# Kernel tuning notes

Measured on AMD Instinct MI355X. Metric: run time of the kernel, lower is better.

The kernel has to match this reference:

```python
import jax, jax.numpy as jnp
import numpy as np

B, C_IN, P, N = 4, 8, 12000, 64
C_PFN = 64          # PFN output channels (hardcoded in source)
H = W = 282         # BEV canvas size (hardcoded)
PILLAR = 0.16       # pillar size in meters
XMIN = YMIN = -22.0 # grid origin (x_edges/y_edges = arange(-22, 22, 0.16))
EPS = 1e-5          # BatchNorm eps (torch default)


def setup_inputs() -> dict:
    key = jax.random.key(0)
    ks = jax.random.split(key, 12)
    # coordinates/features uniform in the grid range so pillars land on the canvas
    sweep = jax.random.uniform(ks[0], (B, C_IN, P, N), jnp.float32, -22.0, 22.0)
    map_in = jax.random.uniform(ks[1], (B, C_IN, P, N), jnp.float32, -22.0, 22.0)
    s = 1.0 / np.sqrt(C_IN)
    w_sweep = jax.random.uniform(ks[2], (C_PFN, C_IN), jnp.float32, -s, s)
    b_sweep = jax.random.uniform(ks[3], (C_PFN,), jnp.float32, -s, s)
    gamma_sweep = 1.0 + 0.1 * jax.random.normal(ks[4], (C_PFN,), jnp.float32)
    beta_sweep = 0.1 * jax.random.normal(ks[5], (C_PFN,), jnp.float32)
    w_map = jax.random.uniform(ks[6], (C_PFN, C_IN), jnp.float32, -s, s)
    b_map = jax.random.uniform(ks[7], (C_PFN,), jnp.float32, -s, s)
    gamma_map = 1.0 + 0.1 * jax.random.normal(ks[8], (C_PFN,), jnp.float32)
    beta_map = 0.1 * jax.random.normal(ks[9], (C_PFN,), jnp.float32)
    sbb = 1.0 / np.sqrt(2 * C_PFN)
    w_bb = jax.random.uniform(ks[10], (C_PFN, 2 * C_PFN), jnp.float32, -sbb, sbb)
    b_bb = jax.random.uniform(ks[11], (C_PFN,), jnp.float32, -sbb, sbb)
    return {"sweep": sweep, "map_in": map_in,
            "w_sweep": w_sweep, "b_sweep": b_sweep,
            "gamma_sweep": gamma_sweep, "beta_sweep": beta_sweep,
            "w_map": w_map, "b_map": b_map,
            "gamma_map": gamma_map, "beta_map": beta_map,
            "w_bb": w_bb, "b_bb": b_bb}


def pfn(x, w, b, gamma, beta):
    # 1x1 conv: [B,8,P,N] -> [B,64,P,N]
    y = jnp.einsum('bcpn,oc->bopn', x, w) + b[None, :, None, None]
    # BatchNorm2d, training-mode batch stats over (B,P,N) per channel
    mean = y.mean(axis=(0, 2, 3), keepdims=True)
    var = y.var(axis=(0, 2, 3), keepdims=True)
    y = (y - mean) * jax.lax.rsqrt(var + EPS)
    y = y * gamma[None, :, None, None] + beta[None, :, None, None]
    y = jax.nn.relu(y)
    return y.max(axis=3)  # max over points -> [B,64,P]


def scatter_to_canvas(inp, feats):
    # inp: [B,8,P,N] (x,y coords at channels 0,1, point 0); feats: [B,64,P]
    x = inp[:, 0, :, 0]  # [B,P]
    y = inp[:, 1, :, 0]
    valid = x != 0  # pillar_list = nonzero(PFN_input[b,0,:,0])
    xg = jnp.clip(jnp.floor((x - XMIN) / PILLAR).astype(jnp.int32), 0, W - 1)
    yg = jnp.clip(jnp.floor((y - YMIN) / PILLAR).astype(jnp.int32), 0, H - 1)
    # route invalid pillars out of bounds so mode='drop' discards them
    xg = jnp.where(valid, xg, W)
    yg = jnp.where(valid, yg, H)
    bidx = jnp.broadcast_to(jnp.arange(B, dtype=jnp.int32)[:, None], (B, P))
    canvas = jnp.zeros((B, H, W, C_PFN), feats.dtype)
    canvas = canvas.at[bidx, yg, xg].set(jnp.swapaxes(feats, 1, 2), mode='drop')
    return jnp.transpose(canvas, (0, 3, 1, 2))  # [B,64,H,W]


def reference(sweep, map_in, w_sweep, b_sweep, gamma_sweep, beta_sweep,
              w_map, b_map, gamma_map, beta_map, w_bb, b_bb):
    sweep_feats = pfn(sweep, w_sweep, b_sweep, gamma_sweep, beta_sweep)
    map_feats = pfn(map_in, w_map, b_map, gamma_map, beta_map)
    sweep_canvas = scatter_to_canvas(sweep, sweep_feats)
    map_canvas = scatter_to_canvas(map_in, map_feats)
    cat = jnp.concatenate([sweep_canvas, map_canvas], axis=1)  # [B,128,H,W]
    # Backbone 1x1 conv (in-channels corrected to 128 to match the data)
    out = jnp.einsum('bchw,oc->bohw', cat, w_bb) + b_bb[None, :, None, None]
    return out
```

## Files before the change

### kernel.cpp

```cpp
#include <hip/hip_runtime.h>
#include <cfloat>
#include <math.h>

namespace {
constexpr int Bn = 4, Cin = 8, Pn = 12000, Nn = 64, Co = 64, Hh = 282, Ww = 282;
constexpr int NPIL  = Bn * Pn;
constexpr int NCELL = Hh * Ww;
constexpr int CHW   = Pn * Nn;
constexpr double CNTD = (double)Bn * Pn * Nn;
constexpr int K1B = 1024;
constexpr int WL_CAP = 48000;
constexpr int APPLY_B = (WL_CAP + 255) / 256;
constexpr int FILL_B = (Bn * Co * NCELL / 4) / 256;

constexpr size_t PAR_OFF  = 0;
constexpr size_t MOM_OFF  = 1024;
constexpr size_t HDR_OFF  = 2048;
constexpr size_t WLS_OFF  = 8192;
constexpr size_t PART_OFF = WLS_OFF;
constexpr size_t WLM_OFF  = WLS_OFF + (size_t)WL_CAP * 8;
constexpr size_t WIN_OFF  = WLM_OFF + (size_t)WL_CAP * 8;
constexpr size_t YMAX_OFF = WIN_OFF + (size_t)2 * Bn * NCELL * 4;
constexpr size_t WS_NEED  = YMAX_OFF + (size_t)2 * NPIL * 64 * 4;

typedef __attribute__((ext_vector_type(8))) float f32x8_t;

__device__ __forceinline__ int cell_of(float xc, float yc) {
  int xg = (int)floorf((xc + 22.0f) * 6.25f);
  int yg = (int)floorf((yc + 22.0f) * 6.25f);
  xg = min(max(xg, 0), Ww - 1);
  yg = min(max(yg, 0), Hh - 1);
  return yg * Ww + xg;
}

__device__ __forceinline__ float firstlane(float v) {
  return __int_as_float(__builtin_amdgcn_readfirstlane(__float_as_int(v)));
}

__device__ __forceinline__ float dpp_xor1(float v) {
  return __int_as_float(__builtin_amdgcn_update_dpp(
      0, __float_as_int(v), 0xB1, 0xF, 0xF, true));
}
__device__ __forceinline__ float dpp_xor2(float v) {
  return __int_as_float(__builtin_amdgcn_update_dpp(
      0, __float_as_int(v), 0x4E, 0xF, 0xF, true));
}
}

__global__ void kdiag(float* __restrict__ out, float v) {
  if (threadIdx.x == 0 && blockIdx.x == 0) out[0] = v;
}

__global__ __launch_bounds__(256) void kinit_fill(
    const float* __restrict__ b_bb, float* __restrict__ out,
    int* __restrict__ winners, int* __restrict__ hdr)
{
  if (blockIdx.x < FILL_B) {
    const int idx = blockIdx.x * 256 + threadIdx.x;
    const int plane = idx / (NCELL / 4);
    const float v = b_bb[plane & 63];
    ((float4*)out)[idx] = make_float4(v, v, v, v);
  } else {
    const int t = (blockIdx.x - FILL_B) * 256 + threadIdx.x;
    if (t < 8) hdr[t] = 0;
    for (int i = t; i < 2 * Bn * NCELL; i += 256 * 256) winners[i] = -1;
  }
}

__global__ __launch_bounds__(256) void k1_momfeat(
    const float* __restrict__ sweep, const float* __restrict__ map_in,
    const float* __restrict__ w_s, const float* __restrict__ b_s,
    const float* __restrict__ w_m, const float* __restrict__ b_m,
    float* __restrict__ partOut, int* __restrict__ winners,
    float* __restrict__ ymax)
{
  __shared__ float red[4][44];
  const int lane = threadIdx.x & 63;
  const int wv   = threadIdx.x >> 6;
  const int bid2 = blockIdx.x & (K1B - 1);
  const int inp  = blockIdx.x / K1B;
  const float* x  = inp ? map_in : sweep;
  const float* w  = inp ? w_m : w_s;
  const float* bb = inp ? b_m : b_s;
  int*   win = winners + inp * Bn * NCELL;
  float* ym  = ymax + (size_t)inp * NPIL * 64;
  const int gw   = (bid2 * 256 + (int)threadIdx.x) >> 6;
  const int nw   = (K1B * 256) >> 6;

  float sacc[8];
  float macc[36];
#pragma unroll
  for (int i = 0; i < 8; ++i) sacc[i] = 0.f;
#pragma unroll
  for (int i = 0; i < 36; ++i) macc[i] = 0.f;

  const int l0 = lane & 1, l1 = (lane >> 1) & 1, l2 = (lane >> 2) & 1;

  for (int pp = gw; pp < NPIL; pp += nw) {
    const int b = pp / Pn;
    const int p = pp - b * Pn;
    const float* xb = x + (size_t)b * Cin * CHW + (size_t)p * Nn + lane;
    float xv[Cin];
#pragma unroll
    for (int c = 0; c < Cin; ++c) xv[c] = xb[(size_t)c * CHW];

#pragma unroll
    for (int c = 0; c < Cin; ++c) sacc[c] += xv[c];
    {
      int k = 0;
#pragma unroll
      for (int i = 0; i < 8; ++i)
#pragma unroll
        for (int j = i; j < 8; ++j) { macc[k] = fmaf(xv[i], xv[j], macc[k]); ++k; }
    }

    const float xc = firstlane(xv[0]);
    if (xc != 0.0f) {
      const float yc = firstlane(xv[1]);
      if (lane == 0) atomicMax(&win[b * NCELL + cell_of(xc, yc)], p);
    }

    float res = 0.f;
#pragma unroll
    for (int g = 0; g < 8; ++g) {
      f32x8_t wr0, wr1, wr2, wr3, wr4, wr5, wr6, wr7, b8;
      asm("s_load_dwordx8 %0, %9, 0x0\n\t"
          "s_load_dwordx8 %1, %9, 0x20\n\t"
          "s_load_dwordx8 %2, %9, 0x40\n\t"
          "s_load_dwordx8 %3, %9, 0x60\n\t"
          "s_load_dwordx8 %4, %9, 0x80\n\t"
          "s_load_dwordx8 %5, %9, 0xA0\n\t"
          "s_load_dwordx8 %6, %9, 0xC0\n\t"
          "s_load_dwordx8 %7, %9, 0xE0\n\t"
          "s_load_dwordx8 %8, %10, 0x0\n\t"
          "s_waitcnt lgkmcnt(0)"
          : "=&s"(wr0), "=&s"(wr1), "=&s"(wr2), "=&s"(wr3), "=&s"(wr4),
            "=&s"(wr5), "=&s"(wr6), "=&s"(wr7), "=&s"(b8)
          : "s"(w + g * 64), "s"(bb + g * 8));

      float z[8];
#define PFN_ROW(J, WR)                                                        \
      {                                                                       \
        float y = b8[J];                                                      \
        _Pragma("unroll")                                                     \
        for (int c = 0; c < Cin; ++c) y = fmaf(WR[c], xv[c], y);              \
        z[J] = y;                                                             \
      }
      PFN_ROW(0, wr0) PFN_ROW(1, wr1) PFN_ROW(2, wr2) PFN_ROW(3, wr3)
      PFN_ROW(4, wr4) PFN_ROW(5, wr5) PFN_ROW(6, wr6) PFN_ROW(7, wr7)
#undef PFN_ROW

      float t0[4];
#pragma unroll
      for (int i = 0; i < 4; ++i) {
        const float send = l0 ? z[2 * i] : z[2 * i + 1];
        const float keep = l0 ? z[2 * i + 1] : z[2 * i];
        t0[i] = fmaxf(keep, dpp_xor1(send));
      }
      float t1[2];
#pragma unroll
      for (int i = 0; i < 2; ++i) {
        const float send = l1 ? t0[2 * i] : t0[2 * i + 1];
        const float keep = l1 ? t0[2 * i + 1] : t0[2 * i];
        t1[i] = fmaxf(keep, dpp_xor2(send));
      }
      {
        const float send = l2 ? t1[0] : t1[1];
        const float keep = l2 ? t1[1] : t1[0];
        float v = fmaxf(keep, __shfl_xor(send, 4, 64));
        v = fmaxf(v, __shfl_xor(v, 8, 64));
        v = fmaxf(v, __shfl_xor(v, 16, 64));
        v = fmaxf(v, __shfl_xor(v, 32, 64));
        if ((lane >> 3) == g) res = v;
      }
    }
    ym[(size_t)pp * 64 + lane] = res;
  }

#pragma unroll
  for (int k = 0; k < 44; ++k) {
    float v = (k < 8) ? sacc[k] : macc[k - 8];
#pragma unroll
    for (int off = 32; off > 0; off >>= 1) v += __shfl_down(v, off, 64);
    if (lane == 0) red[wv][k] = v;
  }
  __syncthreads();
  if (threadIdx.x < 44) {
    const float s = red[0][threadIdx.x] + red[1][threadIdx.x] +
                    red[2][threadIdx.x] + red[3][threadIdx.x];
    partOut[(size_t)bid2 * 88 + inp * 44 + threadIdx.x] = s;
  }
}

__global__ __launch_bounds__(256) void k1b_reduce(
    const float* __restrict__ part, double* __restrict__ mom)
{
  __shared__ double sd[256];
  const int t = blockIdx.x;
  double s = 0.0;
  for (int blk = threadIdx.x; blk < K1B; blk += 256)
    s += (double)part[(size_t)blk * 88 + t];
  sd[threadIdx.x] = s;
  __syncthreads();
  for (int off = 128; off > 0; off >>= 1) {
    if (threadIdx.x < off) sd[threadIdx.x] += sd[threadIdx.x + off];
    __syncthreads();
  }
  if (threadIdx.x == 0) mom[t] = sd[0];
}

__global__ void k2_params(const double* __restrict__ mom,
    const float* __restrict__ w_s, const float* __restrict__ b_s,
    const float* __restrict__ g_s, const float* __restrict__ be_s,
    const float* __restrict__ w_m, const float* __restrict__ b_m,
    const float* __restrict__ g_m, const float* __restrict__ be_m,
    float* __restrict__ par, int* __restrict__ hdr)
{
  const int t = threadIdx.x;
  if (t >= 128) return;
  const int inp = t >> 6, o = t & 63;
  const double* m = mom + inp * 44;
  const float* w    = (inp ? w_m : w_s) + o * Cin;
  const float bias  = (inp ? b_m : b_s)[o];
  const float gamma = (inp ? g_m : g_s)[o];
  const float beta  = (inp ? be_m : be_s)[o];
  double S[8];
#pragma unroll
  for (int c = 0; c < 8; ++c) S[c] = m[c] / CNTD;
  double mean = (double)bias;
#pragma unroll
  for (int c = 0; c < 8; ++c) mean += (double)w[c] * S[c];
  double var = 0.0;
  int k = 8;
#pragma unroll
  for (int i = 0; i < 8; ++i)
#pragma unroll
    for (int j = i; j < 8; ++j) {
      const double cov = m[k] / CNTD - S[i] * S[j];
      const double ww = (double)w[i] * (double)w[j];
      var += (i == j ? ww : 2.0 * ww) * cov;
      ++k;
    }
  const double a = (double)gamma / sqrt(var + 1e-5);
  const double c = (double)beta - mean * a;
  const float af = (float)a;
  par[inp * 128 + o]      = af;
  par[inp * 128 + 64 + o] = (float)c;
  if (af < 0.f) atomicOr(&hdr[4 + inp * 2 + (o >> 5)], 1 << (o & 31));
}

__global__ __launch_bounds__(256) void k_negfix(
    const float* __restrict__ sweep, const float* __restrict__ map_in,
    const float* __restrict__ w_s, const float* __restrict__ b_s,
    const float* __restrict__ w_m, const float* __restrict__ b_m,
    const int* __restrict__ hdr, float* __restrict__ ymax)
{
  const int inp = blockIdx.x & 1;
  const unsigned m0 = (unsigned)hdr[4 + inp * 2];
  const unsigned m1 = (unsigned)hdr[5 + inp * 2];
  if ((m0 | m1) == 0u) return;
  const float* x  = inp ? map_in : sweep;
  const float* w  = inp ? w_m : w_s;
  const float* bb = inp ? b_m : b_s;
  float* ym = ymax + (size_t)inp * NPIL * 64;
  const int lane = threadIdx.x & 63;
  const int wv   = threadIdx.x >> 6;
  const int gw   = (int)(blockIdx.x >> 1) * 4 + wv;
  const int nw   = (int)(gridDim.x >> 1) * 4;
  for (int pp = gw; pp < NPIL; pp += nw) {
    const int b = pp / Pn;
    const int p = pp - b * Pn;
    const size_t base = (size_t)b * Cin * CHW + (size_t)p * Nn;
    float xv[Cin];
#pragma unroll
    for (int c = 0; c < Cin; ++c) xv[c] = x[base + (size_t)c * CHW + lane];
    for (int half = 0; half < 2; ++half) {
      unsigned m = half ? m1 : m0;
      while (m) {
        const int bit = __ffs(m) - 1;
        m &= m - 1;
        const int o = half * 32 + bit;
        float y = bb[o];
#pragma unroll
        for (int c = 0; c < Cin; ++c) y = fmaf(w[o * Cin + c], xv[c], y);
#pragma unroll
        for (int s = 1; s < 64; s <<= 1) y = fminf(y, __shfl_xor(y, s, 64));
        if (lane == 0) ym[(size_t)pp * 64 + o] = y;
      }
    }
  }
}

__global__ __launch_bounds__(256) void k_compact(
    const int* __restrict__ winners, int* __restrict__ hdr,
    int2* __restrict__ wlS, int2* __restrict__ wlM)
{
  __shared__ int cS[4], cM[4];
  __shared__ int baseS, baseM;
  const int t = blockIdx.x * 256 + threadIdx.x;
  const int lane = threadIdx.x & 63;
  const int wv   = threadIdx.x >> 6;
  int ps = -1, pm = -1, outbase = 0, b = 0;
  if (t < Bn * NCELL) {
    b = t / NCELL;
    const int hw = t - b * NCELL;
    outbase = b * Co * NCELL + hw;
    ps = winners[t];
    pm = winners[Bn * NCELL + t];
  }
  const unsigned long long ms = __ballot(ps >= 0);
  const unsigned long long mm = __ballot(pm >= 0);
  if (lane == 0) { cS[wv] = __popcll(ms); cM[wv] = __popcll(mm); }
  __syncthreads();
  if (threadIdx.x == 0) {
    const int c = cS[0] + cS[1] + cS[2] + cS[3];
    baseS = c ? atomicAdd(&hdr[1], c) : 0;
  } else if (threadIdx.x == 64) {
    const int c = cM[0] + cM[1] + cM[2] + cM[3];
    baseM = c ? atomicAdd(&hdr[2], c) : 0;
  }
  __syncthreads();
  const unsigned long long below = (1ull << lane) - 1ull;
  if (ps >= 0) {
    int off = baseS + __popcll(ms & below);
    for (int w2 = 0; w2 < wv; ++w2) off += cS[w2];
    wlS[off] = make_int2(outbase, b * Pn + ps);
  }
  if (pm >= 0) {
    int off = baseM + __popcll(mm & below);
    for (int w2 = 0; w2 < wv; ++w2) off += cM[w2];
    wlM[off] = make_int2(outbase, b * Pn + pm);
  }
}

template<int WHICH>
__global__ __launch_bounds__(256) void k_apply(
    const int* __restrict__ hdr, const int2* __restrict__ wl,
    const float* __restrict__ ymax, const float* __restrict__ par,
    const float* __restrict__ w_bb, const float* __restrict__ b_bb,
    float* __restrict__ out)
{
  __shared__ float4 wlds[Co * 16];
  __shared__ float bbb[Co];
  __shared__ float av[Co], cv[Co];
  for (int i = threadIdx.x; i < Co * 16; i += 256)
    wlds[i] = ((const float4*)w_bb)[((i >> 4) << 5) + (WHICH ? 16 : 0) + (i & 15)];
  if (threadIdx.x < Co) {
    bbb[threadIdx.x] = b_bb[threadIdx.x];
    av[threadIdx.x]  = par[WHICH * 128 + threadIdx.x];
    cv[threadIdx.x]  = par[WHICH * 128 + 64 + threadIdx.x];
  }
  __syncthreads();
  const float* ybase = ymax + (size_t)WHICH * NPIL * 64;
  const int cnt = hdr[1 + WHICH];
  for (int i = blockIdx.x * blockDim.x + threadIdx.x; i < cnt;
       i += gridDim.x * blockDim.x) {
    const int2 e = wl[i];
    const float4* yp = (const float4*)(ybase + (size_t)e.y * 64);
    float4 f[16];
#pragma unroll
    for (int k = 0; k < 16; ++k) {
      const float4 ymv = yp[k];
      f[k].x = fmaxf(fmaf(av[4 * k + 0], ymv.x, cv[4 * k + 0]), 0.f);
      f[k].y = fmaxf(fmaf(av[4 * k + 1], ymv.y, cv[4 * k + 1]), 0.f);
      f[k].z = fmaxf(fmaf(av[4 * k + 2], ymv.z, cv[4 * k + 2]), 0.f);
      f[k].w = fmaxf(fmaf(av[4 * k + 3], ymv.w, cv[4 * k + 3]), 0.f);
    }
    float* op = out + e.x;
#pragma unroll 2
    for (int o = 0; o < Co; ++o) {
      float acc = WHICH ? op[(size_t)o * NCELL] : bbb[o];
      const float4* row = &wlds[o * 16];
#pragma unroll
      for (int k = 0; k < 16; ++k) {
        const float4 w4 = row[k];
        acc = fmaf(w4.x, f[k].x, acc); acc = fmaf(w4.y, f[k].y, acc);
        acc = fmaf(w4.z, f[k].z, acc); acc = fmaf(w4.w, f[k].w, acc);
      }
      op[(size_t)o * NCELL] = acc;
    }
  }
}

__global__ void k6_verdict(const int* __restrict__ hdr, float* __restrict__ out)
{
  if (threadIdx.x != 0 || blockIdx.x != 0) return;
  const int n_occ = hdr[1] + hdr[2];
  if (n_occ < 80000 || n_occ > 96000) out[0] = 1.0e7f + (float)n_occ;
}

extern "C" void kernel_launch(void* const* d_in, const int* in_sizes, int n_in,
                              void* d_out, int out_size, void* d_ws, size_t ws_size,
                              hipStream_t stream)
{
  const float* sweep  = (const float*)d_in[0];
  const float* map_in = (const float*)d_in[1];
  const float* w_s  = (const float*)d_in[2];
  const float* b_s  = (const float*)d_in[3];
  const float* g_s  = (const float*)d_in[4];
  const float* be_s = (const float*)d_in[5];
  const float* w_m  = (const float*)d_in[6];
  const float* b_m  = (const float*)d_in[7];
  const float* g_m  = (const float*)d_in[8];
  const float* be_m = (const float*)d_in[9];
  const float* w_bb = (const float*)d_in[10];
  const float* b_bb = (const float*)d_in[11];
  float* out = (float*)d_out;

  const int exp_sz[12] = {24576000, 24576000, 512, 64, 64, 64, 512, 64, 64, 64, 8192, 64};
  int bad_idx = -1;
  if (n_in != 12) bad_idx = 11;
  else for (int i = 0; i < 12; ++i) if (in_sizes[i] != exp_sz[i]) { bad_idx = i; break; }
  if (bad_idx >= 0) {
    kdiag<<<1, 1, 0, stream>>>(out, 9.0e7f + 1.0e5f * (float)bad_idx);
    return;
  }
  if (ws_size < WS_NEED) {
    kdiag<<<1, 1, 0, stream>>>(out, 8.0e7f);
    return;
  }

  char* ws = (char*)d_ws;
  float*  par     = (float*)(ws + PAR_OFF);
  double* mom     = (double*)(ws + MOM_OFF);
  int*    hdr     = (int*)(ws + HDR_OFF);
  int*    winners = (int*)(ws + WIN_OFF);
  float*  ymax    = (float*)(ws + YMAX_OFF);
  float*  part    = (float*)(ws + PART_OFF);
  int2*   wlS     = (int2*)(ws + WLS_OFF);
  int2*   wlM     = (int2*)(ws + WLM_OFF);

  kinit_fill<<<FILL_B + 256, 256, 0, stream>>>(b_bb, out, winners, hdr);
  k1_momfeat<<<2 * K1B, 256, 0, stream>>>(sweep, map_in, w_s, b_s, w_m, b_m,
                                          part, winners, ymax);
  k1b_reduce<<<88, 256, 0, stream>>>(part, mom);
  k2_params<<<1, 128, 0, stream>>>(mom, w_s, b_s, g_s, be_s, w_m, b_m, g_m, be_m,
                                   par, hdr);
  k_negfix<<<1024, 256, 0, stream>>>(sweep, map_in, w_s, b_s, w_m, b_m, hdr, ymax);
  k_compact<<<(Bn * NCELL + 255) / 256, 256, 0, stream>>>(winners, hdr, wlS, wlM);
  k_apply<0><<<APPLY_B, 256, 0, stream>>>(hdr, wlS, ymax, par, w_bb, b_bb, out);
  k_apply<1><<<APPLY_B, 256, 0, stream>>>(hdr, wlM, ymax, par, w_bb, b_bb, out);
  k6_verdict<<<1, 1, 0, stream>>>(hdr, out);
}
```

Baseline: 329.8 us.

## Split feature max into separate kernel computing only winning pillars

```diff
diff --git a/kernel.cpp b/kernel.cpp
--- a/kernel.cpp
+++ b/kernel.cpp
@@ -36,15 +36,6 @@
 __device__ __forceinline__ float firstlane(float v) {
   return __int_as_float(__builtin_amdgcn_readfirstlane(__float_as_int(v)));
 }
-
-__device__ __forceinline__ float dpp_xor1(float v) {
-  return __int_as_float(__builtin_amdgcn_update_dpp(
-      0, __float_as_int(v), 0xB1, 0xF, 0xF, true));
-}
-__device__ __forceinline__ float dpp_xor2(float v) {
-  return __int_as_float(__builtin_amdgcn_update_dpp(
-      0, __float_as_int(v), 0x4E, 0xF, 0xF, true));
-}
 }
 
 __global__ void kdiag(float* __restrict__ out, float v) {
@@ -67,23 +58,17 @@
   }
 }
 
-__global__ __launch_bounds__(256) void k1_momfeat(
+__global__ __launch_bounds__(256) void k1_mom(
     const float* __restrict__ sweep, const float* __restrict__ map_in,
-    const float* __restrict__ w_s, const float* __restrict__ b_s,
-    const float* __restrict__ w_m, const float* __restrict__ b_m,
-    float* __restrict__ partOut, int* __restrict__ winners,
-    float* __restrict__ ymax)
+    float* __restrict__ partOut, int* __restrict__ winners)
 {
   __shared__ float red[4][44];
   const int lane = threadIdx.x & 63;
   const int wv   = threadIdx.x >> 6;
   const int bid2 = blockIdx.x & (K1B - 1);
   const int inp  = blockIdx.x / K1B;
-  const float* x  = inp ? map_in : sweep;
-  const float* w  = inp ? w_m : w_s;
-  const float* bb = inp ? b_m : b_s;
-  int*   win = winners + inp * Bn * NCELL;
-  float* ym  = ymax + (size_t)inp * NPIL * 64;
+  const float* x = inp ? map_in : sweep;
+  int* win = winners + inp * Bn * NCELL;
   const int gw   = (bid2 * 256 + (int)threadIdx.x) >> 6;
   const int nw   = (K1B * 256) >> 6;
 
@@ -93,8 +78,6 @@
   for (int i = 0; i < 8; ++i) sacc[i] = 0.f;
 #pragma unroll
   for (int i = 0; i < 36; ++i) macc[i] = 0.f;
-
-  const int l0 = lane & 1, l1 = (lane >> 1) & 1, l2 = (lane >> 2) & 1;
 
   for (int pp = gw; pp < NPIL; pp += nw) {
     const int b = pp / Pn;
@@ -103,7 +86,6 @@
     float xv[Cin];
 #pragma unroll
     for (int c = 0; c < Cin; ++c) xv[c] = xb[(size_t)c * CHW];
-
 #pragma unroll
     for (int c = 0; c < Cin; ++c) sacc[c] += xv[c];
     {
@@ -113,68 +95,11 @@
 #pragma unroll
         for (int j = i; j < 8; ++j) { macc[k] = fmaf(xv[i], xv[j], macc[k]); ++k; }
     }
-
     const float xc = firstlane(xv[0]);
     if (xc != 0.0f) {
       const float yc = firstlane(xv[1]);
       if (lane == 0) atomicMax(&win[b * NCELL + cell_of(xc, yc)], p);
     }
-
-    float res = 0.f;
-#pragma unroll
-    for (int g = 0; g < 8; ++g) {
-      f32x8_t wr0, wr1, wr2, wr3, wr4, wr5, wr6, wr7, b8;
-      asm("s_load_dwordx8 %0, %9, 0x0\n\t"
-          "s_load_dwordx8 %1, %9, 0x20\n\t"
-          "s_load_dwordx8 %2, %9, 0x40\n\t"
-          "s_load_dwordx8 %3, %9, 0x60\n\t"
-          "s_load_dwordx8 %4, %9, 0x80\n\t"
-          "s_load_dwordx8 %5, %9, 0xA0\n\t"
-          "s_load_dwordx8 %6, %9, 0xC0\n\t"
-          "s_load_dwordx8 %7, %9, 0xE0\n\t"
-          "s_load_dwordx8 %8, %10, 0x0\n\t"
-          "s_waitcnt lgkmcnt(0)"
-          : "=&s"(wr0), "=&s"(wr1), "=&s"(wr2), "=&s"(wr3), "=&s"(wr4),
-            "=&s"(wr5), "=&s"(wr6), "=&s"(wr7), "=&s"(b8)
-          : "s"(w + g * 64), "s"(bb + g * 8));
-
-      float z[8];
-#define PFN_ROW(J, WR)                                                        \
-      {                                                                       \
-        float y = b8[J];                                                      \
-        _Pragma("unroll")                                                     \
-        for (int c = 0; c < Cin; ++c) y = fmaf(WR[c], xv[c], y);              \
-        z[J] = y;                                                             \
-      }
-      PFN_ROW(0, wr0) PFN_ROW(1, wr1) PFN_ROW(2, wr2) PFN_ROW(3, wr3)
-      PFN_ROW(4, wr4) PFN_ROW(5, wr5) PFN_ROW(6, wr6) PFN_ROW(7, wr7)
-#undef PFN_ROW
-
-      float t0[4];
-#pragma unroll
-      for (int i = 0; i < 4; ++i) {
-        const float send = l0 ? z[2 * i] : z[2 * i + 1];
-        const float keep = l0 ? z[2 * i + 1] : z[2 * i];
-        t0[i] = fmaxf(keep, dpp_xor1(send));
-      }
-      float t1[2];
-#pragma unroll
-      for (int i = 0; i < 2; ++i) {
-        const float send = l1 ? t0[2 * i] : t0[2 * i + 1];
-        const float keep = l1 ? t0[2 * i + 1] : t0[2 * i];
-        t1[i] = fmaxf(keep, dpp_xor2(send));
-      }
-      {
-        const float send = l2 ? t1[0] : t1[1];
-        const float keep = l2 ? t1[1] : t1[0];
-        float v = fmaxf(keep, __shfl_xor(send, 4, 64));
-        v = fmaxf(v, __shfl_xor(v, 8, 64));
-        v = fmaxf(v, __shfl_xor(v, 16, 64));
-        v = fmaxf(v, __shfl_xor(v, 32, 64));
-        if ((lane >> 3) == g) res = v;
-      }
-    }
-    ym[(size_t)pp * 64 + lane] = res;
   }
 
 #pragma unroll
@@ -247,6 +172,122 @@
   par[inp * 128 + o]      = af;
   par[inp * 128 + 64 + o] = (float)c;
   if (af < 0.f) atomicOr(&hdr[4 + inp * 2 + (o >> 5)], 1 << (o & 31));
+}
+
+__global__ __launch_bounds__(256) void k5f_feat(
+    const float* __restrict__ sweep, const float* __restrict__ map_in,
+    const float* __restrict__ w_s, const float* __restrict__ b_s,
+    const float* __restrict__ w_m, const float* __restrict__ b_m,
+    const int* __restrict__ winners, float* __restrict__ ymax)
+{
+  const int lane = threadIdx.x & 63;
+  const int wv   = __builtin_amdgcn_readfirstlane(threadIdx.x >> 6);
+  int pp = blockIdx.x * 4 + wv;
+  const int inp = (pp >= NPIL) ? 1 : 0;
+  pp -= inp * NPIL;
+  const float* x  = inp ? map_in : sweep;
+  const float* w  = inp ? w_m : w_s;
+  const float* bb = inp ? b_m : b_s;
+  const int* win  = winners + inp * Bn * NCELL;
+  float* ym = ymax + (size_t)inp * NPIL * 64;
+
+  const int b = pp / Pn;
+  const int p = pp - b * Pn;
+  const int base32 = __builtin_amdgcn_readfirstlane(b * (Cin * CHW) + p * Nn);
+  const float* xb = x + base32;
+  const float* xp0 = xb;
+  const float* xp1 = xb + CHW;
+  const float* xp2 = xb + 2 * CHW;
+  const float* xp3 = xb + 3 * CHW;
+  const float* xp4 = xb + 4 * CHW;
+  const float* xp5 = xb + 5 * CHW;
+  const float* xp6 = xb + 6 * CHW;
+  const float* xp7 = xb + 7 * CHW;
+
+#define LOADGRP(S0, S1, S2, S3, S4, S5, S6, S7, OFF)                          \
+  asm("s_load_dwordx8 %0, %8, %c16\n\t"                                       \
+      "s_load_dwordx8 %1, %9, %c16\n\t"                                       \
+      "s_load_dwordx8 %2, %10, %c16\n\t"                                      \
+      "s_load_dwordx8 %3, %11, %c16\n\t"                                      \
+      "s_load_dwordx8 %4, %12, %c16\n\t"                                      \
+      "s_load_dwordx8 %5, %13, %c16\n\t"                                      \
+      "s_load_dwordx8 %6, %14, %c16\n\t"                                      \
+      "s_load_dwordx8 %7, %15, %c16\n\t"                                      \
+      "s_waitcnt lgkmcnt(0)"                                                  \
+      : "=&s"(S0), "=&s"(S1), "=&s"(S2), "=&s"(S3),                           \
+        "=&s"(S4), "=&s"(S5), "=&s"(S6), "=&s"(S7)                            \
+      : "s"(xp0), "s"(xp1), "s"(xp2), "s"(xp3),                               \
+        "s"(xp4), "s"(xp5), "s"(xp6), "s"(xp7), "n"(OFF))
+
+#define COMPGRP(S0, S1, S2, S3, S4, S5, S6, S7)                               \
+  _Pragma("unroll")                                                           \
+  for (int n = 0; n < 8; ++n) {                                               \
+    float y = breg;                                                           \
+    y = fmaf(wreg[0], S0[n], y);                                              \
+    y = fmaf(wreg[1], S1[n], y);                                              \
+    y = fmaf(wreg[2], S2[n], y);                                              \
+    y = fmaf(wreg[3], S3[n], y);                                              \
+    y = fmaf(wreg[4], S4[n], y);                                              \
+    y = fmaf(wreg[5], S5[n], y);                                              \
+    y = fmaf(wreg[6], S6[n], y);                                              \
+    y = fmaf(wreg[7], S7[n], y);                                              \
+    m = fmaxf(m, y);                                                          \
+  }
+
+  f32x8_t s0, s1, s2, s3, s4, s5, s6, s7;
+  LOADGRP(s0, s1, s2, s3, s4, s5, s6, s7, 0);
+  const float xcv = s0[0];
+  if (xcv == 0.0f) return;
+  const float ycv = s1[0];
+  const int cell = cell_of(xcv, ycv);
+  if (win[b * NCELL + cell] != p) return;
+
+  const float breg = bb[lane];
+  float wreg[Cin];
+#pragma unroll
+  for (int c = 0; c < Cin; ++c) wreg[c] = w[lane * Cin + c];
+
+  float m = -FLT_MAX;
+  COMPGRP(s0, s1, s2, s3, s4, s5, s6, s7);
+  {
+    f32x8_t t0, t1, t2, t3, t4, t5, t6, t7;
+    LOADGRP(t0, t1, t2, t3, t4, t5, t6, t7, 32);
+    COMPGRP(t0, t1, t2, t3, t4, t5, t6, t7);
+  }
+  {
+    f32x8_t t0, t1, t2, t3, t4, t5, t6, t7;
+    LOADGRP(t0, t1, t2, t3, t4, t5, t6, t7, 64);
+    COMPGRP(t0, t1, t2, t3, t4, t5, t6, t7);
+  }
+  {
+    f32x8_t t0, t1, t2, t3, t4, t5, t6, t7;
+    LOADGRP(t0, t1, t2, t3, t4, t5, t6, t7, 96);
+    COMPGRP(t0, t1, t2, t3, t4, t5, t6, t7);
+  }
+  {
+    f32x8_t t0, t1, t2, t3, t4, t5, t6, t7;
+    LOADGRP(t0, t1, t2, t3, t4, t5, t6, t7, 128);
+    COMPGRP(t0, t1, t2, t3, t4, t5, t6, t7);
+  }
+  {
+    f32x8_t t0, t1, t2, t3, t4, t5, t6, t7;
+    LOADGRP(t0, t1, t2, t3, t4, t5, t6, t7, 160);
+    COMPGRP(t0, t1, t2, t3, t4, t5, t6, t7);
+  }
+  {
+    f32x8_t t0, t1, t2, t3, t4, t5, t6, t7;
+    LOADGRP(t0, t1, t2, t3, t4, t5, t6, t7, 192);
+    COMPGRP(t0, t1, t2, t3, t4, t5, t6, t7);
+  }
+  {
+    f32x8_t t0, t1, t2, t3, t4, t5, t6, t7;
+    LOADGRP(t0, t1, t2, t3, t4, t5, t6, t7, 224);
+    COMPGRP(t0, t1, t2, t3, t4, t5, t6, t7);
+  }
+#undef LOADGRP
+#undef COMPGRP
+
+  ym[(size_t)pp * 64 + lane] = m;
 }
 
 __global__ __launch_bounds__(256) void k_negfix(
@@ -431,13 +472,14 @@
   int2*   wlM     = (int2*)(ws + WLM_OFF);
 
   kinit_fill<<<FILL_B + 256, 256, 0, stream>>>(b_bb, out, winners, hdr);
-  k1_momfeat<<<2 * K1B, 256, 0, stream>>>(sweep, map_in, w_s, b_s, w_m, b_m,
-                                          part, winners, ymax);
+  k1_mom<<<2 * K1B, 256, 0, stream>>>(sweep, map_in, part, winners);
   k1b_reduce<<<88, 256, 0, stream>>>(part, mom);
   k2_params<<<1, 128, 0, stream>>>(mom, w_s, b_s, g_s, be_s, w_m, b_m, g_m, be_m,
                                    par, hdr);
+  k_compact<<<(Bn * NCELL + 255) / 256, 256, 0, stream>>>(winners, hdr, wlS, wlM);
+  k5f_feat<<<2 * NPIL / 4, 256, 0, stream>>>(sweep, map_in, w_s, b_s, w_m, b_m,
+                                             winners, ymax);
   k_negfix<<<1024, 256, 0, stream>>>(sweep, map_in, w_s, b_s, w_m, b_m, hdr, ymax);
-  k_compact<<<(Bn * NCELL + 255) / 256, 256, 0, stream>>>(winners, hdr, wlS, wlM);
   k_apply<0><<<APPLY_B, 256, 0, stream>>>(hdr, wlS, ymax, par, w_bb, b_bb, out);
   k_apply<1><<<APPLY_B, 256, 0, stream>>>(hdr, wlM, ymax, par, w_bb, b_bb, out);
   k6_verdict<<<1, 1, 0, stream>>>(hdr, out);
```

After: 361.1 us. 9.5% more time.

## Merge kernels to cut launch count and overlap output fill with moment pass

Applied to the files above, without the earlier changes.

```diff
diff --git a/kernel.cpp b/kernel.cpp
--- a/kernel.cpp
+++ b/kernel.cpp
@@ -12,9 +12,10 @@
 constexpr int WL_CAP = 48000;
 constexpr int APPLY_B = (WL_CAP + 255) / 256;
 constexpr int FILL_B = (Bn * Co * NCELL / 4) / 256;
+constexpr int NEGB = 1024;
+constexpr int COMPACT_B = (Bn * NCELL + 255) / 256;
 
 constexpr size_t PAR_OFF  = 0;
-constexpr size_t MOM_OFF  = 1024;
 constexpr size_t HDR_OFF  = 2048;
 constexpr size_t WLS_OFF  = 8192;
 constexpr size_t PART_OFF = WLS_OFF;
@@ -51,34 +52,34 @@
   if (threadIdx.x == 0 && blockIdx.x == 0) out[0] = v;
 }
 
-__global__ __launch_bounds__(256) void kinit_fill(
+__global__ void k0_init(int* __restrict__ winners, int* __restrict__ hdr) {
+  const int stride = gridDim.x * blockDim.x;
+  const int t = blockIdx.x * blockDim.x + threadIdx.x;
+  if (t < 8) hdr[t] = 0;
+  for (int i = t; i < 2 * Bn * NCELL; i += stride) winners[i] = -1;
+}
+
+__global__ __launch_bounds__(256) void k_mega(
+    const float* __restrict__ sweep, const float* __restrict__ map_in,
+    const float* __restrict__ w_s, const float* __restrict__ b_s,
+    const float* __restrict__ w_m, const float* __restrict__ b_m,
     const float* __restrict__ b_bb, float* __restrict__ out,
-    int* __restrict__ winners, int* __restrict__ hdr)
+    float* __restrict__ partOut, int* __restrict__ winners,
+    float* __restrict__ ymax)
 {
   if (blockIdx.x < FILL_B) {
     const int idx = blockIdx.x * 256 + threadIdx.x;
     const int plane = idx / (NCELL / 4);
     const float v = b_bb[plane & 63];
     ((float4*)out)[idx] = make_float4(v, v, v, v);
-  } else {
-    const int t = (blockIdx.x - FILL_B) * 256 + threadIdx.x;
-    if (t < 8) hdr[t] = 0;
-    for (int i = t; i < 2 * Bn * NCELL; i += 256 * 256) winners[i] = -1;
-  }
-}
-
-__global__ __launch_bounds__(256) void k1_momfeat(
-    const float* __restrict__ sweep, const float* __restrict__ map_in,
-    const float* __restrict__ w_s, const float* __restrict__ b_s,
-    const float* __restrict__ w_m, const float* __restrict__ b_m,
-    float* __restrict__ partOut, int* __restrict__ winners,
-    float* __restrict__ ymax)
-{
+    return;
+  }
   __shared__ float red[4][44];
+  const int bid  = blockIdx.x - FILL_B;
   const int lane = threadIdx.x & 63;
   const int wv   = threadIdx.x >> 6;
-  const int bid2 = blockIdx.x & (K1B - 1);
-  const int inp  = blockIdx.x / K1B;
+  const int bid2 = bid & (K1B - 1);
+  const int inp  = bid / K1B;
   const float* x  = inp ? map_in : sweep;
   const float* w  = inp ? w_m : w_s;
   const float* bb = inp ? b_m : b_s;
@@ -192,34 +193,31 @@
   }
 }
 
-__global__ __launch_bounds__(256) void k1b_reduce(
-    const float* __restrict__ part, double* __restrict__ mom)
-{
-  __shared__ double sd[256];
-  const int t = blockIdx.x;
-  double s = 0.0;
-  for (int blk = threadIdx.x; blk < K1B; blk += 256)
-    s += (double)part[(size_t)blk * 88 + t];
-  sd[threadIdx.x] = s;
-  __syncthreads();
-  for (int off = 128; off > 0; off >>= 1) {
-    if (threadIdx.x < off) sd[threadIdx.x] += sd[threadIdx.x + off];
-    __syncthreads();
-  }
-  if (threadIdx.x == 0) mom[t] = sd[0];
-}
-
-__global__ void k2_params(const double* __restrict__ mom,
+__global__ __launch_bounds__(512) void k1b2_params(
+    const float* __restrict__ part,
     const float* __restrict__ w_s, const float* __restrict__ b_s,
     const float* __restrict__ g_s, const float* __restrict__ be_s,
     const float* __restrict__ w_m, const float* __restrict__ b_m,
     const float* __restrict__ g_m, const float* __restrict__ be_m,
     float* __restrict__ par, int* __restrict__ hdr)
 {
-  const int t = threadIdx.x;
-  if (t >= 128) return;
-  const int inp = t >> 6, o = t & 63;
-  const double* m = mom + inp * 44;
+  __shared__ double sd[88][4];
+  __shared__ double smom[88];
+  const int tid = threadIdx.x;
+  if (tid < 352) {
+    const int c = tid >> 2, q = tid & 3;
+    double s = 0.0;
+    for (int j = 0; j < K1B / 4; ++j)
+      s += (double)part[(size_t)(q * (K1B / 4) + j) * 88 + c];
+    sd[c][q] = s;
+  }
+  __syncthreads();
+  if (tid < 88)
+    smom[tid] = (sd[tid][0] + sd[tid][1]) + (sd[tid][2] + sd[tid][3]);
+  __syncthreads();
+  if (tid >= 128) return;
+  const int inp = tid >> 6, o = tid & 63;
+  const double* m = smom + inp * 44;
   const float* w    = (inp ? w_m : w_s) + o * Cin;
   const float bias  = (inp ? b_m : b_s)[o];
   const float gamma = (inp ? g_m : g_s)[o];
@@ -249,12 +247,54 @@
   if (af < 0.f) atomicOr(&hdr[4 + inp * 2 + (o >> 5)], 1 << (o & 31));
 }
 
-__global__ __launch_bounds__(256) void k_negfix(
+__global__ __launch_bounds__(256) void k_negfix_compact(
     const float* __restrict__ sweep, const float* __restrict__ map_in,
     const float* __restrict__ w_s, const float* __restrict__ b_s,
     const float* __restrict__ w_m, const float* __restrict__ b_m,
-    const int* __restrict__ hdr, float* __restrict__ ymax)
+    const int* __restrict__ winners, int* __restrict__ hdr,
+    int2* __restrict__ wlS, int2* __restrict__ wlM,
+    float* __restrict__ ymax)
 {
+  if (blockIdx.x >= NEGB) {
+    __shared__ int cS[4], cM[4];
+    __shared__ int baseS, baseM;
+    const int t = (blockIdx.x - NEGB) * 256 + threadIdx.x;
+    const int lane = threadIdx.x & 63;
+    const int wvc  = threadIdx.x >> 6;
+    int ps = -1, pm = -1, outbase = 0, b = 0;
+    if (t < Bn * NCELL) {
+      b = t / NCELL;
+      const int hw = t - b * NCELL;
+      outbase = b * Co * NCELL + hw;
+      ps = winners[t];
+      pm = winners[Bn * NCELL + t];
+    }
+    const unsigned long long ms = __ballot(ps >= 0);
+    const unsigned long long mm = __ballot(pm >= 0);
+    if (lane == 0) { cS[wvc] = __popcll(ms); cM[wvc] = __popcll(mm); }
+    __syncthreads();
+    if (threadIdx.x == 0) {
+      const int c = cS[0] + cS[1] + cS[2] + cS[3];
+      baseS = c ? atomicAdd(&hdr[1], c) : 0;
+    } else if (threadIdx.x == 64) {
+      const int c = cM[0] + cM[1] + cM[2] + cM[3];
+      baseM = c ? atomicAdd(&hdr[2], c) : 0;
+    }
+    __syncthreads();
+    const unsigned long long below = (1ull << lane) - 1ull;
+    if (ps >= 0) {
+      int off = baseS + __popcll(ms & below);
+      for (int w2 = 0; w2 < wvc; ++w2) off += cS[w2];
+      wlS[off] = make_int2(outbase, b * Pn + ps);
+    }
+    if (pm >= 0) {
+      int off = baseM + __popcll(mm & below);
+      for (int w2 = 0; w2 < wvc; ++w2) off += cM[w2];
+      wlM[off] = make_int2(outbase, b * Pn + pm);
+    }
+    return;
+  }
+
   const int inp = blockIdx.x & 1;
   const unsigned m0 = (unsigned)hdr[4 + inp * 2];
   const unsigned m1 = (unsigned)hdr[5 + inp * 2];
@@ -266,7 +306,7 @@
   const int lane = threadIdx.x & 63;
   const int wv   = threadIdx.x >> 6;
   const int gw   = (int)(blockIdx.x >> 1) * 4 + wv;
-  const int nw   = (int)(gridDim.x >> 1) * 4;
+  const int nw   = (NEGB >> 1) * 4;
   for (int pp = gw; pp < NPIL; pp += nw) {
     const int b = pp / Pn;
     const int p = pp - b * Pn;
@@ -288,48 +328,6 @@
         if (lane == 0) ym[(size_t)pp * 64 + o] = y;
       }
     }
-  }
-}
-
-__global__ __launch_bounds__(256) void k_compact(
-    const int* __restrict__ winners, int* __restrict__ hdr,
-    int2* __restrict__ wlS, int2* __restrict__ wlM)
-{
-  __shared__ int cS[4], cM[4];
-  __shared__ int baseS, baseM;
-  const int t = blockIdx.x * 256 + threadIdx.x;
-  const int lane = threadIdx.x & 63;
-  const int wv   = threadIdx.x >> 6;
-  int ps = -1, pm = -1, outbase = 0, b = 0;
-  if (t < Bn * NCELL) {
-    b = t / NCELL;
-    const int hw = t - b * NCELL;
-    outbase = b * Co * NCELL + hw;
-    ps = winners[t];
-    pm = winners[Bn * NCELL + t];
-  }
-  const unsigned long long ms = __ballot(ps >= 0);
-  const unsigned long long mm = __ballot(pm >= 0);
-  if (lane == 0) { cS[wv] = __popcll(ms); cM[wv] = __popcll(mm); }
-  __syncthreads();
-  if (threadIdx.x == 0) {
-    const int c = cS[0] + cS[1] + cS[2] + cS[3];
-    baseS = c ? atomicAdd(&hdr[1], c) : 0;
-  } else if (threadIdx.x == 64) {
-    const int c = cM[0] + cM[1] + cM[2] + cM[3];
-    baseM = c ? atomicAdd(&hdr[2], c) : 0;
-  }
-  __syncthreads();
-  const unsigned long long below = (1ull << lane) - 1ull;
-  if (ps >= 0) {
-    int off = baseS + __popcll(ms & below);
-    for (int w2 = 0; w2 < wv; ++w2) off += cS[w2];
-    wlS[off] = make_int2(outbase, b * Pn + ps);
-  }
-  if (pm >= 0) {
-    int off = baseM + __popcll(mm & below);
-    for (int w2 = 0; w2 < wv; ++w2) off += cM[w2];
-    wlM[off] = make_int2(outbase, b * Pn + pm);
   }
 }
 
@@ -380,13 +378,10 @@
       op[(size_t)o * NCELL] = acc;
     }
   }
-}
-
-__global__ void k6_verdict(const int* __restrict__ hdr, float* __restrict__ out)
-{
-  if (threadIdx.x != 0 || blockIdx.x != 0) return;
-  const int n_occ = hdr[1] + hdr[2];
-  if (n_occ < 80000 || n_occ > 96000) out[0] = 1.0e7f + (float)n_occ;
+  if (WHICH == 1 && blockIdx.x == 0 && threadIdx.x == 0) {
+    const int n_occ = hdr[1] + hdr[2];
+    if (n_occ < 80000 || n_occ > 96000) out[0] = 1.0e7f + (float)n_occ;
+  }
 }
 
 extern "C" void kernel_launch(void* const* d_in, const int* in_sizes, int n_in,
@@ -422,7 +417,6 @@
 
   char* ws = (char*)d_ws;
   float*  par     = (float*)(ws + PAR_OFF);
-  double* mom     = (double*)(ws + MOM_OFF);
   int*    hdr     = (int*)(ws + HDR_OFF);
   int*    winners = (int*)(ws + WIN_OFF);
   float*  ymax    = (float*)(ws + YMAX_OFF);
@@ -430,15 +424,13 @@
   int2*   wlS     = (int2*)(ws + WLS_OFF);
   int2*   wlM     = (int2*)(ws + WLM_OFF);
 
-  kinit_fill<<<FILL_B + 256, 256, 0, stream>>>(b_bb, out, winners, hdr);
-  k1_momfeat<<<2 * K1B, 256, 0, stream>>>(sweep, map_in, w_s, b_s, w_m, b_m,
-                                          part, winners, ymax);
-  k1b_reduce<<<88, 256, 0, stream>>>(part, mom);
-  k2_params<<<1, 128, 0, stream>>>(mom, w_s, b_s, g_s, be_s, w_m, b_m, g_m, be_m,
-                                   par, hdr);
-  k_negfix<<<1024, 256, 0, stream>>>(sweep, map_in, w_s, b_s, w_m, b_m, hdr, ymax);
-  k_compact<<<(Bn * NCELL + 255) / 256, 256, 0, stream>>>(winners, hdr, wlS, wlM);
+  k0_init<<<512, 256, 0, stream>>>(winners, hdr);
+  k_mega<<<FILL_B + 2 * K1B, 256, 0, stream>>>(sweep, map_in, w_s, b_s, w_m, b_m,
+                                               b_bb, out, part, winners, ymax);
+  k1b2_params<<<1, 512, 0, stream>>>(part, w_s, b_s, g_s, be_s,
+                                     w_m, b_m, g_m, be_m, par, hdr);
+  k_negfix_compact<<<NEGB + COMPACT_B, 256, 0, stream>>>(
+      sweep, map_in, w_s, b_s, w_m, b_m, winners, hdr, wlS, wlM, ymax);
   k_apply<0><<<APPLY_B, 256, 0, stream>>>(hdr, wlS, ymax, par, w_bb, b_bb, out);
   k_apply<1><<<APPLY_B, 256, 0, stream>>>(hdr, wlM, ymax, par, w_bb, b_bb, out);
-  k6_verdict<<<1, 1, 0, stream>>>(hdr, out);
-}
+}
```

Measured after the change: 331.2 us. No clear change (+0.4%).
